# Performance work log

Hardware: AMD Instinct MI355X
Metric: run time of the kernel (lower is better)

Reference implementation:

```python
import jax, jax.numpy as jnp
import numpy as np

B, S, D, E, F = 4, 2048, 1024, 8, 4096


def setup_inputs() -> dict:
    key = jax.random.key(0)
    k1, k2, k3, k4 = jax.random.split(key, 4)
    x = jax.random.normal(k1, (B, S, D), dtype=jnp.float32)
    Wg = jax.random.normal(k2, (D, E), dtype=jnp.float32) / np.sqrt(D).astype(np.float32)
    w1 = jax.random.normal(k3, (E, D, F), dtype=jnp.float32) / np.sqrt(D).astype(np.float32)
    w2 = jax.random.normal(k4, (E, F, D), dtype=jnp.float32) / np.sqrt(F).astype(np.float32)
    return {"x": x, "Wg": Wg, "w1": w1, "w2": w2, "k": 2}


def reference(x, Wg, w1, w2, k):
    # x: [B, S, D] -> flatten tokens
    b, s, d = x.shape
    e = Wg.shape[1]
    xf = x.reshape(-1, d)                      # [T, D]
    t = xf.shape[0]
    logits = xf @ Wg                           # [T, E] gate logits
    topv, topi = jax.lax.top_k(logits, k)      # [T, k]
    # softmax over the top-k logits in float32, cast back (matches torch impl)
    w = jax.nn.softmax(topv.astype(jnp.float32), axis=-1).astype(x.dtype)
    # dense routing matrix [T, E]: weight for selected experts, 0 elsewhere
    route = jnp.zeros((t, e), dtype=x.dtype).at[jnp.arange(t)[:, None], topi].set(w)
    # per-expert FFN: y_e = gelu(x @ w1[e]) @ w2[e]; combine = sum_e route[:,e] * y_e
    out = jnp.zeros_like(xf)
    for ei in range(e):  # small fixed expert count
        h = jax.nn.gelu(xf @ w1[ei])           # [T, F]
        out = out + route[:, ei:ei + 1] * (h @ w2[ei])
    return out.reshape(b, s, d)
```

## Files before the change

kernel.cpp:

```cpp
#include <hip/hip_runtime.h>
#include <stdint.h>

#define T_TOK   8192
#define DMODEL  1024
#define NEXP    8
#define FFN     4096
#define TASSIGN 16384

typedef unsigned short u16;
typedef __attribute__((ext_vector_type(8))) short short8;
typedef __attribute__((ext_vector_type(8))) u16 u16x8;
typedef __attribute__((ext_vector_type(4))) u16 u16x4;
typedef __attribute__((ext_vector_type(4))) float f32x4;

__device__ __forceinline__ float bf2f(u16 u) {
  union { unsigned int i; float f; } v; v.i = ((unsigned int)u) << 16; return v.f;
}
__device__ __forceinline__ u16 f2bf(float f) {
  union { float f; unsigned int i; } v; v.f = f;
  unsigned int x = v.i;
  x += 0x7fffu + ((x >> 16) & 1u);
  return (u16)(x >> 16);
}
__device__ __forceinline__ float gelu_tanh(float x) {
  float z = 0.7978845608028654f * x * (1.0f + 0.044715f * x * x);
  float t = 1.0f - 2.0f / (__expf(2.0f * z) + 1.0f);
  return 0.5f * x * (1.0f + t);
}
__device__ __forceinline__ void async16(const void* g, void* l) {
  __builtin_amdgcn_global_load_lds((__attribute__((address_space(1))) void*)g,
                                   (__attribute__((address_space(3))) void*)l,
                                   16, 0, 0);
}

__global__ void init_kernel(int* __restrict__ meta) {
  if (threadIdx.x < 32) meta[threadIdx.x] = 0;
}

__global__ void gate_kernel(const float* __restrict__ x, const float* __restrict__ Wg,
                            int* __restrict__ topi, float* __restrict__ topw,
                            int* __restrict__ counts, u16* __restrict__ xb) {
  __shared__ float sWg[DMODEL * NEXP];
  int tid = threadIdx.x;
  for (int i = tid; i < DMODEL * NEXP / 4; i += 256)
    ((float4*)sWg)[i] = ((const float4*)Wg)[i];
  __syncthreads();

  int wave = tid >> 6, lane = tid & 63;
  int t = blockIdx.x * 4 + wave;

  float acc[NEXP] = {0, 0, 0, 0, 0, 0, 0, 0};
  const float* xr = x + (size_t)t * DMODEL;
  u16* xbr = xb + (size_t)t * DMODEL;
  for (int d0 = 0; d0 < DMODEL; d0 += 128) {
    int d = d0 + lane * 2;
    float2 xx = *(const float2*)(xr + d);
    *(uint32_t*)(xbr + d) = (uint32_t)f2bf(xx.x) | ((uint32_t)f2bf(xx.y) << 16);
    const float* g0 = sWg + (size_t)d * NEXP;
#pragma unroll
    for (int e = 0; e < NEXP; e++)
      acc[e] += xx.x * g0[e] + xx.y * g0[NEXP + e];
  }
#pragma unroll
  for (int off = 32; off > 0; off >>= 1)
#pragma unroll
    for (int e = 0; e < NEXP; e++)
      acc[e] += __shfl_xor(acc[e], off, 64);

  if (lane == 0) {
    float v0 = -1e30f, v1 = -1e30f; int i0 = 0, i1 = 0;
#pragma unroll
    for (int e = 0; e < NEXP; e++) {
      float v = acc[e];
      if (v > v0) { v1 = v0; i1 = i0; v0 = v; i0 = e; }
      else if (v > v1) { v1 = v; i1 = e; }
    }
    float e1 = __expf(v1 - v0);
    float s = 1.0f / (1.0f + e1);
    topi[t * 2] = i0; topi[t * 2 + 1] = i1;
    topw[t * 2] = s;  topw[t * 2 + 1] = e1 * s;
    atomicAdd(&counts[i0], 1);
    atomicAdd(&counts[i1], 1);
  }
}

__global__ void scan_kernel(const int* __restrict__ counts, int* __restrict__ offsets,
                            int* __restrict__ cursors) {
  if (threadIdx.x == 0) {
    int s = 0;
    for (int e = 0; e < NEXP; e++) { offsets[e] = s; s += counts[e]; }
    offsets[NEXP] = s;
  }
  if (threadIdx.x < NEXP) cursors[threadIdx.x] = 0;
}

__global__ void build_kernel(const int* __restrict__ topi, const int* __restrict__ offsets,
                             int* __restrict__ cursors, int* __restrict__ perm,
                             int* __restrict__ slotrow) {
  int t = blockIdx.x * blockDim.x + threadIdx.x;
  if (t >= T_TOK) return;
#pragma unroll
  for (int s = 0; s < 2; s++) {
    int e = topi[t * 2 + s];
    int p = atomicAdd(&cursors[e], 1);
    int g = offsets[e] + p;
    perm[g] = t;
    slotrow[t * 2 + s] = g;
  }
}

__global__ void transpose_kernel(const float* __restrict__ w1, const float* __restrict__ w2,
                                 u16* __restrict__ w1t, u16* __restrict__ w2t) {
  __shared__ u16 sh[64][72];
  int z = blockIdx.y;
  const float* src; u16* dst; int R, C;
  if (z < 8) { src = w1 + (size_t)z * (DMODEL * FFN); dst = w1t + (size_t)z * (FFN * DMODEL); R = DMODEL; C = FFN; }
  else       { src = w2 + (size_t)(z - 8) * (FFN * DMODEL); dst = w2t + (size_t)(z - 8) * (DMODEL * FFN); R = FFN; C = DMODEL; }
  int tilesC = C >> 6;
  int rt = blockIdx.x / tilesC, ct = blockIdx.x % tilesC;
  int tid = threadIdx.x;
#pragma unroll
  for (int i = 0; i < 2; i++) {
    int idx = i * 256 + tid;
    int r = idx >> 3, c8 = (idx & 7) * 8;
    const float* s = src + (size_t)(rt * 64 + r) * C + ct * 64 + c8;
    float4 v0 = *(const float4*)s, v1 = *(const float4*)(s + 4);
    u16* d = &sh[r][c8];
    d[0] = f2bf(v0.x); d[1] = f2bf(v0.y); d[2] = f2bf(v0.z); d[3] = f2bf(v0.w);
    d[4] = f2bf(v1.x); d[5] = f2bf(v1.y); d[6] = f2bf(v1.z); d[7] = f2bf(v1.w);
  }
  __syncthreads();
#pragma unroll
  for (int i = 0; i < 2; i++) {
    int idx = i * 256 + tid;
    int c = idx >> 3, r8 = (idx & 7) * 8;
    u16x8 v;
#pragma unroll
    for (int j = 0; j < 8; j++) v[j] = sh[r8 + j][c];
    *(u16x8*)(dst + (size_t)(ct * 64 + c) * R + rt * 64 + r8) = v;
  }
}

template <int K, int N, bool GATHER, bool GELU>
__global__ __launch_bounds__(256) void gemm_t_kernel(
    const u16* __restrict__ A, const u16* __restrict__ Bt, u16* __restrict__ C,
    const int* __restrict__ offsets, const int* __restrict__ perm) {
  __shared__ u16 As[128 * 32];
  __shared__ u16 Bs[128 * 32];
  int e = blockIdx.z;
  int off = offsets[e];
  int nrows = offsets[e + 1] - off;
  int mtile = blockIdx.y;
  if (mtile * 128 >= nrows) return;
  int ntile = blockIdx.x;

  int tid = threadIdx.x;
  int wave = tid >> 6, lane = tid & 63;

  int rr = tid >> 2;
  int kc = (tid & 3) * 8;

  int m0 = mtile * 128 + rr;
  int mm0 = min(m0, nrows - 1);
  int mm1 = min(m0 + 64, nrows - 1);
  const u16 *arow0, *arow1;
  if (GATHER) {
    arow0 = A + (size_t)perm[off + mm0] * K + kc;
    arow1 = A + (size_t)perm[off + mm1] * K + kc;
  } else {
    arow0 = A + (size_t)(off + mm0) * K + kc;
    arow1 = A + (size_t)(off + mm1) * K + kc;
  }
  const u16* bbase = Bt + (size_t)e * ((size_t)N * K);
  const u16* brow0 = bbase + (size_t)(ntile * 128 + rr) * K + kc;
  const u16* brow1 = bbase + (size_t)(ntile * 128 + rr + 64) * K + kc;

  u16* asd0 = As + (size_t)(wave * 64) * 8;
  u16* asd1 = As + (size_t)(256 + wave * 64) * 8;
  u16* bsd0 = Bs + (size_t)(wave * 64) * 8;
  u16* bsd1 = Bs + (size_t)(256 + wave * 64) * 8;

  int wm = (wave >> 1) * 64, wn = (wave & 1) * 64;
  int lm = lane & 15, kq = lane >> 4;

  f32x4 acc[4][4];
  f32x4 zero = {0.f, 0.f, 0.f, 0.f};
#pragma unroll
  for (int i = 0; i < 4; i++)
#pragma unroll
    for (int j = 0; j < 4; j++) acc[i][j] = zero;

  for (int k0 = 0; k0 < K; k0 += 32) {
    async16(arow0 + k0, asd0);
    async16(arow1 + k0, asd1);
    async16(brow0 + k0, bsd0);
    async16(brow1 + k0, bsd1);
    __syncthreads();
    short8 a[4], b[4];
#pragma unroll
    for (int i = 0; i < 4; i++) {
      a[i] = *(const short8*)(As + (size_t)(wm + i * 16 + lm) * 32 + kq * 8);
      b[i] = *(const short8*)(Bs + (size_t)(wn + i * 16 + lm) * 32 + kq * 8);
    }
#pragma unroll
    for (int i = 0; i < 4; i++)
#pragma unroll
      for (int j = 0; j < 4; j++)
        acc[i][j] = __builtin_amdgcn_mfma_f32_16x16x32_bf16(a[i], b[j], acc[i][j], 0, 0, 0);
    __syncthreads();
  }

#pragma unroll
  for (int i = 0; i < 4; i++) {
    int rbase = mtile * 128 + wm + i * 16 + kq * 4;
#pragma unroll
    for (int r = 0; r < 4; r++) {
      int row = rbase + r;
      if (row < nrows) {
        u16* crow = C + (size_t)(off + row) * N + ntile * 128 + wn + lm;
#pragma unroll
        for (int j = 0; j < 4; j++) {
          float v = acc[i][j][r];
          if (GELU) v = gelu_tanh(v);
          crow[j * 16] = f2bf(v);
        }
      }
    }
  }
}

template <int K, int N, bool GATHER, bool GELU>
__global__ __launch_bounds__(256) void gemm_f_kernel(
    const u16* __restrict__ A, const float* __restrict__ B, u16* __restrict__ C,
    const int* __restrict__ offsets, const int* __restrict__ perm) {
  __shared__ u16 As[128 * 32];
  __shared__ u16 Bs[128 * 32];
  int e = blockIdx.z;
  int off = offsets[e];
  int nrows = offsets[e + 1] - off;
  int mtile = blockIdx.y;
  if (mtile * 128 >= nrows) return;
  int ntile = blockIdx.x;

  int tid = threadIdx.x;
  int wave = tid >> 6, lane = tid & 63;

  int rr = tid >> 2;
  int kc = (tid & 3) * 8;
  int m0 = mtile * 128 + rr;
  int mm0 = min(m0, nrows - 1);
  int mm1 = min(m0 + 64, nrows - 1);
  const u16 *arow0, *arow1;
  if (GATHER) {
    arow0 = A + (size_t)perm[off + mm0] * K + kc;
    arow1 = A + (size_t)perm[off + mm1] * K + kc;
  } else {
    arow0 = A + (size_t)(off + mm0) * K + kc;
    arow1 = A + (size_t)(off + mm1) * K + kc;
  }

  int kk2 = (tid >> 4) * 2;
  int n8  = (tid & 15) * 8;
  const float* brow0 = B + (size_t)e * ((size_t)K * N) + (size_t)kk2 * N
                         + (size_t)ntile * 128 + n8;
  const float* brow1 = brow0 + N;

  int wm = (wave >> 1) * 64, wn = (wave & 1) * 64;
  int lm = lane & 15, kq = lane >> 4;

  f32x4 acc[4][4];
  f32x4 zero = {0.f, 0.f, 0.f, 0.f};
#pragma unroll
  for (int i = 0; i < 4; i++)
#pragma unroll
    for (int j = 0; j < 4; j++) acc[i][j] = zero;

  uint32_t* bs32 = (uint32_t*)Bs;
  for (int k0 = 0; k0 < K; k0 += 32) {
    u16x8 av0 = *(const u16x8*)(arow0 + k0);
    u16x8 av1 = *(const u16x8*)(arow1 + k0);
    float4 b00 = *(const float4*)(brow0 + (size_t)k0 * N);
    float4 b01 = *(const float4*)(brow0 + (size_t)k0 * N + 4);
    float4 b10 = *(const float4*)(brow1 + (size_t)k0 * N);
    float4 b11 = *(const float4*)(brow1 + (size_t)k0 * N + 4);
    __syncthreads();
    *(u16x8*)(As + (size_t)rr * 32 + kc) = av0;
    *(u16x8*)(As + (size_t)(rr + 64) * 32 + kc) = av1;
    int wcol = kk2 >> 1;
    bs32[(size_t)(n8 + 0) * 16 + wcol] = (uint32_t)f2bf(b00.x) | ((uint32_t)f2bf(b10.x) << 16);
    bs32[(size_t)(n8 + 1) * 16 + wcol] = (uint32_t)f2bf(b00.y) | ((uint32_t)f2bf(b10.y) << 16);
    bs32[(size_t)(n8 + 2) * 16 + wcol] = (uint32_t)f2bf(b00.z) | ((uint32_t)f2bf(b10.z) << 16);
    bs32[(size_t)(n8 + 3) * 16 + wcol] = (uint32_t)f2bf(b00.w) | ((uint32_t)f2bf(b10.w) << 16);
    bs32[(size_t)(n8 + 4) * 16 + wcol] = (uint32_t)f2bf(b01.x) | ((uint32_t)f2bf(b11.x) << 16);
    bs32[(size_t)(n8 + 5) * 16 + wcol] = (uint32_t)f2bf(b01.y) | ((uint32_t)f2bf(b11.y) << 16);
    bs32[(size_t)(n8 + 6) * 16 + wcol] = (uint32_t)f2bf(b01.z) | ((uint32_t)f2bf(b11.z) << 16);
    bs32[(size_t)(n8 + 7) * 16 + wcol] = (uint32_t)f2bf(b01.w) | ((uint32_t)f2bf(b11.w) << 16);
    __syncthreads();
    short8 a[4], b[4];
#pragma unroll
    for (int i = 0; i < 4; i++) {
      a[i] = *(const short8*)(As + (size_t)(wm + i * 16 + lm) * 32 + kq * 8);
      b[i] = *(const short8*)(Bs + (size_t)(wn + i * 16 + lm) * 32 + kq * 8);
    }
#pragma unroll
    for (int i = 0; i < 4; i++)
#pragma unroll
      for (int j = 0; j < 4; j++)
        acc[i][j] = __builtin_amdgcn_mfma_f32_16x16x32_bf16(a[i], b[j], acc[i][j], 0, 0, 0);
  }

#pragma unroll
  for (int i = 0; i < 4; i++) {
    int rbase = mtile * 128 + wm + i * 16 + kq * 4;
#pragma unroll
    for (int r = 0; r < 4; r++) {
      int row = rbase + r;
      if (row < nrows) {
        u16* crow = C + (size_t)(off + row) * N + ntile * 128 + wn + lm;
#pragma unroll
        for (int j = 0; j < 4; j++) {
          float v = acc[i][j][r];
          if (GELU) v = gelu_tanh(v);
          crow[j * 16] = f2bf(v);
        }
      }
    }
  }
}

__global__ void combine_kernel(const u16* __restrict__ Y, const int* __restrict__ slotrow,
                               const float* __restrict__ topw, float* __restrict__ out) {
  int idx = blockIdx.x * 256 + threadIdx.x;
  int t = idx >> 8;
  int c = (idx & 255) * 4;
  int g0 = slotrow[t * 2], g1 = slotrow[t * 2 + 1];
  float w0 = topw[t * 2], w1 = topw[t * 2 + 1];
  u16x4 y0 = *(const u16x4*)(Y + (size_t)g0 * DMODEL + c);
  u16x4 y1 = *(const u16x4*)(Y + (size_t)g1 * DMODEL + c);
  float4 o;
  o.x = w0 * bf2f(y0[0]) + w1 * bf2f(y1[0]);
  o.y = w0 * bf2f(y0[1]) + w1 * bf2f(y1[1]);
  o.z = w0 * bf2f(y0[2]) + w1 * bf2f(y1[2]);
  o.w = w0 * bf2f(y0[3]) + w1 * bf2f(y1[3]);
  *(float4*)(out + (size_t)t * DMODEL + c) = o;
}

extern "C" void kernel_launch(void* const* d_in, const int* in_sizes, int n_in,
                              void* d_out, int out_size, void* d_ws, size_t ws_size,
                              hipStream_t stream) {
  const float* x  = (const float*)d_in[0];
  const float* Wg = (const float*)d_in[1];
  const float* w1 = (const float*)d_in[2];
  const float* w2 = (const float*)d_in[3];
  float* out = (float*)d_out;

  const size_t SZ_H   = (size_t)TASSIGN * FFN * 2;
  const size_t SZ_W1T = (size_t)NEXP * FFN * DMODEL * 2;
  const size_t SZ_W2T = (size_t)NEXP * DMODEL * FFN * 2;
  const size_t SZ_XB  = (size_t)T_TOK * DMODEL * 2;
  const size_t SZ_Y   = (size_t)TASSIGN * DMODEL * 2;
  const size_t SZ_SMALL = (size_t)TASSIGN * 4 * 4 + 4096;
  const size_t WS_FULL = SZ_H + SZ_W1T + SZ_W2T + SZ_XB + SZ_SMALL;

  uint8_t* ws = (uint8_t*)d_ws;
  bool fast = (ws_size >= WS_FULL);

  size_t o = 0;
  u16* H = (u16*)(ws + o); o += SZ_H;
  u16 *w1t = nullptr, *w2t = nullptr, *Y;
  if (fast) {
    w1t = (u16*)(ws + o); o += SZ_W1T;
    w2t = (u16*)(ws + o); o += SZ_W2T;
    Y = w1t;
  } else {
    Y = (u16*)(ws + o); o += SZ_Y;
  }
  u16* xb = (u16*)(ws + o); o += SZ_XB;
  int*   topi    = (int*)(ws + o);   o += (size_t)TASSIGN * 4;
  float* topw    = (float*)(ws + o); o += (size_t)TASSIGN * 4;
  int*   perm    = (int*)(ws + o);   o += (size_t)TASSIGN * 4;
  int*   slotrow = (int*)(ws + o);   o += (size_t)TASSIGN * 4;
  int*   meta    = (int*)(ws + o);
  int* counts = meta, *offsets = meta + 8, *cursors = meta + 17;

  init_kernel<<<1, 64, 0, stream>>>(meta);
  gate_kernel<<<T_TOK / 4, 256, 0, stream>>>(x, Wg, topi, topw, counts, xb);
  scan_kernel<<<1, 64, 0, stream>>>(counts, offsets, cursors);
  build_kernel<<<T_TOK / 256, 256, 0, stream>>>(topi, offsets, cursors, perm, slotrow);

  if (fast) {
    transpose_kernel<<<dim3(1024, 16), 256, 0, stream>>>(w1, w2, w1t, w2t);
    gemm_t_kernel<DMODEL, FFN, true, true>
        <<<dim3(FFN / 128, 64, NEXP), 256, 0, stream>>>(xb, w1t, H, offsets, perm);
    gemm_t_kernel<FFN, DMODEL, false, false>
        <<<dim3(DMODEL / 128, 64, NEXP), 256, 0, stream>>>(H, w2t, Y, offsets, perm);
  } else {
    gemm_f_kernel<DMODEL, FFN, true, true>
        <<<dim3(FFN / 128, 64, NEXP), 256, 0, stream>>>(xb, w1, H, offsets, perm);
    gemm_f_kernel<FFN, DMODEL, false, false>
        <<<dim3(DMODEL / 128, 64, NEXP), 256, 0, stream>>>(H, w2, Y, offsets, perm);
  }
  combine_kernel<<<(T_TOK * DMODEL / 4) / 256, 256, 0, stream>>>(Y, slotrow, topw, out);
}
```

Baseline: 1.041 ms.

## Replace expert GEMM with 256x256 double-buffered pipelined 8-wave kernel

Replaces the 128x128, single-buffered expert GEMM with a 512-thread kernel that computes 256x256 tiles over a K step of 64. Global-to-LDS async loads are double-buffered and interleaved with MFMA phases. LDS is XOR-swizzled to avoid bank conflicts, and s_setprio is raised around the MFMA blocks. The grid is flattened with the expert index in the low bits so experts interleave across CUs. This targets the load-then-sync stall and low arithmetic intensity of the old kernel, at the cost of 128KB of LDS per block, high register pressure and intricate hand scheduling of waitcnt and barriers.

```diff
diff --git a/kernel.cpp b/kernel.cpp
--- a/kernel.cpp
+++ b/kernel.cpp
@@ -142,91 +142,140 @@
 }
 
 template <int K, int N, bool GATHER, bool GELU>
-__global__ __launch_bounds__(256) void gemm_t_kernel(
+__global__ __launch_bounds__(512, 2) void gemm8_kernel(
     const u16* __restrict__ A, const u16* __restrict__ Bt, u16* __restrict__ C,
     const int* __restrict__ offsets, const int* __restrict__ perm) {
-  __shared__ u16 As[128 * 32];
-  __shared__ u16 Bs[128 * 32];
-  int e = blockIdx.z;
+  __shared__ u16 S[65536];
+  constexpr int NTT = N / 256;
+  constexpr int MT  = 32;
+  constexpr int NKT = K / 64;
+
+  int p = blockIdx.x;
+  int e = p & 7;
+  int slot = p >> 3;
+  int ntile = slot / MT;
+  int mtile = slot % MT;
+
   int off = offsets[e];
   int nrows = offsets[e + 1] - off;
-  int mtile = blockIdx.y;
-  if (mtile * 128 >= nrows) return;
-  int ntile = blockIdx.x;
+  if (mtile * 256 >= nrows) return;
 
   int tid = threadIdx.x;
-  int wave = tid >> 6, lane = tid & 63;
-
-  int rr = tid >> 2;
-  int kc = (tid & 3) * 8;
-
-  int m0 = mtile * 128 + rr;
-  int mm0 = min(m0, nrows - 1);
-  int mm1 = min(m0 + 64, nrows - 1);
-  const u16 *arow0, *arow1;
-  if (GATHER) {
-    arow0 = A + (size_t)perm[off + mm0] * K + kc;
-    arow1 = A + (size_t)perm[off + mm1] * K + kc;
-  } else {
-    arow0 = A + (size_t)(off + mm0) * K + kc;
-    arow1 = A + (size_t)(off + mm1) * K + kc;
-  }
+  int w = tid >> 6, l = tid & 63;
+  int lm = l & 15, kq = l >> 4;
+  int warp_m = w >> 2, warp_n = w & 3;
+  int xr = ((l >> 2) & 1) << 4;
+
+  int scol8 = ((l & 7) ^ (((l >> 5) & 1) << 1)) * 8;
+  int rbase = w * 8 + (l >> 3);
+  const u16* aptr[2][2];
+  const u16* bptr[2][2];
   const u16* bbase = Bt + (size_t)e * ((size_t)N * K);
-  const u16* brow0 = bbase + (size_t)(ntile * 128 + rr) * K + kc;
-  const u16* brow1 = bbase + (size_t)(ntile * 128 + rr + 64) * K + kc;
-
-  u16* asd0 = As + (size_t)(wave * 64) * 8;
-  u16* asd1 = As + (size_t)(256 + wave * 64) * 8;
-  u16* bsd0 = Bs + (size_t)(wave * 64) * 8;
-  u16* bsd1 = Bs + (size_t)(256 + wave * 64) * 8;
-
-  int wm = (wave >> 1) * 64, wn = (wave & 1) * 64;
-  int lm = lane & 15, kq = lane >> 4;
-
-  f32x4 acc[4][4];
+#pragma unroll
+  for (int q = 0; q < 2; q++)
+#pragma unroll
+    for (int i = 0; i < 2; i++) {
+      int rr = rbase + i * 64;
+      int rowA = (rr < 64 ? rr : rr + 64) + q * 64;
+      int gm = mtile * 256 + rowA;
+      int gmc = min(gm, nrows - 1);
+      int arow = GATHER ? perm[off + gmc] : (off + gmc);
+      aptr[q][i] = A + (size_t)arow * K + scol8;
+      int rowB = ((rr >> 5) << 6) + (rr & 31) + q * 32;
+      bptr[q][i] = bbase + (size_t)(ntile * 256 + rowB) * K + scol8;
+    }
+  int arb = w * 8;
+  int brb = (w & 3) * 8 + (w >> 2) * 64;
+  u16* As_lds = S;
+  u16* Bs_lds = S + 32768;
+
+#define STAGE_A(q, buf, kt) do {                                                       \
+    async16(aptr[q][0] + (kt) * 64, As_lds + (buf) * 16384 + (arb + (q) * 64) * 64);   \
+    async16(aptr[q][1] + (kt) * 64, As_lds + (buf) * 16384 + (arb + 128 + (q) * 64) * 64); \
+  } while (0)
+#define STAGE_B(q, buf, kt) do {                                                       \
+    async16(bptr[q][0] + (kt) * 64, Bs_lds + (buf) * 16384 + (brb + (q) * 32) * 64);   \
+    async16(bptr[q][1] + (kt) * 64, Bs_lds + (buf) * 16384 + (brb + 128 + (q) * 32) * 64); \
+  } while (0)
+
+  f32x4 acc[8][4];
   f32x4 zero = {0.f, 0.f, 0.f, 0.f};
 #pragma unroll
-  for (int i = 0; i < 4; i++)
+  for (int i = 0; i < 8; i++)
 #pragma unroll
     for (int j = 0; j < 4; j++) acc[i][j] = zero;
 
-  for (int k0 = 0; k0 < K; k0 += 32) {
-    async16(arow0 + k0, asd0);
-    async16(arow1 + k0, asd1);
-    async16(brow0 + k0, bsd0);
-    async16(brow1 + k0, bsd1);
-    __syncthreads();
-    short8 a[4], b[4];
-#pragma unroll
-    for (int i = 0; i < 4; i++) {
-      a[i] = *(const short8*)(As + (size_t)(wm + i * 16 + lm) * 32 + kq * 8);
-      b[i] = *(const short8*)(Bs + (size_t)(wn + i * 16 + lm) * 32 + kq * 8);
-    }
-#pragma unroll
-    for (int i = 0; i < 4; i++)
-#pragma unroll
-      for (int j = 0; j < 4; j++)
-        acc[i][j] = __builtin_amdgcn_mfma_f32_16x16x32_bf16(a[i], b[j], acc[i][j], 0, 0, 0);
-    __syncthreads();
-  }
-
-#pragma unroll
-  for (int i = 0; i < 4; i++) {
-    int rbase = mtile * 128 + wm + i * 16 + kq * 4;
+#define GEMM8_PHASE(BUF, QM, QN, STAGE_STMT, DO_VM)                                    \
+  {                                                                                    \
+    short8 af[4][2], bf[2][2];                                                         \
+    const u16* ab = As_lds + (BUF) * 16384;                                            \
+    const u16* bb = Bs_lds + (BUF) * 16384;                                            \
+    _Pragma("unroll") for (int fi = 0; fi < 4; fi++) {                                 \
+      int ml = warp_m * 128 + ((QM) * 4 + fi) * 16 + lm;                               \
+      _Pragma("unroll") for (int ks = 0; ks < 2; ks++)                                 \
+        af[fi][ks] = *(const short8*)(ab + ((ml * 64 + ks * 32 + kq * 8) ^ xr));       \
+    }                                                                                  \
+    _Pragma("unroll") for (int fj = 0; fj < 2; fj++) {                                 \
+      int nl = warp_n * 64 + ((QN) * 2 + fj) * 16 + lm;                                \
+      _Pragma("unroll") for (int ks = 0; ks < 2; ks++)                                 \
+        bf[fj][ks] = *(const short8*)(bb + ((nl * 64 + ks * 32 + kq * 8) ^ xr));       \
+    }                                                                                  \
+    STAGE_STMT;                                                                        \
+    __builtin_amdgcn_s_barrier();                                                      \
+    asm volatile("s_waitcnt lgkmcnt(0)" ::: "memory");                                 \
+    __builtin_amdgcn_sched_barrier(0);                                                 \
+    __builtin_amdgcn_s_setprio(1);                                                     \
+    _Pragma("unroll") for (int fi = 0; fi < 4; fi++)                                   \
+      _Pragma("unroll") for (int fj = 0; fj < 2; fj++)                                 \
+        _Pragma("unroll") for (int ks = 0; ks < 2; ks++)                               \
+          acc[(QM) * 4 + fi][(QN) * 2 + fj] = __builtin_amdgcn_mfma_f32_16x16x32_bf16( \
+              af[fi][ks], bf[fj][ks], acc[(QM) * 4 + fi][(QN) * 2 + fj], 0, 0, 0);     \
+    __builtin_amdgcn_s_setprio(0);                                                     \
+    if (DO_VM) asm volatile("s_waitcnt vmcnt(4)" ::: "memory");                        \
+    __builtin_amdgcn_s_barrier();                                                      \
+  }
+
+  STAGE_A(0, 0, 0); STAGE_B(0, 0, 0); STAGE_A(1, 0, 0); STAGE_B(1, 0, 0);
+  STAGE_A(0, 1, 1); STAGE_B(0, 1, 1);
+  asm volatile("s_waitcnt vmcnt(4)" ::: "memory");
+  __builtin_amdgcn_s_barrier();
+
+  for (int it = 0; it < NKT / 2; it++) {
+    int kt1 = 2 * it + 1;
+    int t2 = min(2 * it + 2, NKT - 1);
+    int t3 = min(2 * it + 3, NKT - 1);
+    GEMM8_PHASE(0, 0, 0, STAGE_A(1, 1, kt1), 0)
+    GEMM8_PHASE(0, 0, 1, STAGE_B(1, 1, kt1), 0)
+    GEMM8_PHASE(0, 1, 0, STAGE_A(0, 0, t2), 0)
+    GEMM8_PHASE(0, 1, 1, STAGE_B(0, 0, t2), 1)
+    GEMM8_PHASE(1, 0, 0, STAGE_A(1, 0, t2), 0)
+    GEMM8_PHASE(1, 0, 1, STAGE_B(1, 0, t2), 0)
+    GEMM8_PHASE(1, 1, 0, STAGE_A(0, 1, t3), 0)
+    GEMM8_PHASE(1, 1, 1, STAGE_B(0, 1, t3), 1)
+  }
+
+  asm volatile("s_waitcnt vmcnt(0)" ::: "memory");
+
+#pragma unroll
+  for (int fi = 0; fi < 8; fi++) {
+    int rowb = mtile * 256 + warp_m * 128 + fi * 16 + kq * 4;
 #pragma unroll
     for (int r = 0; r < 4; r++) {
-      int row = rbase + r;
+      int row = rowb + r;
       if (row < nrows) {
-        u16* crow = C + (size_t)(off + row) * N + ntile * 128 + wn + lm;
-#pragma unroll
-        for (int j = 0; j < 4; j++) {
-          float v = acc[i][j][r];
+        u16* crow = C + (size_t)(off + row) * N + ntile * 256 + warp_n * 64 + lm;
+#pragma unroll
+        for (int fj = 0; fj < 4; fj++) {
+          float v = acc[fi][fj][r];
           if (GELU) v = gelu_tanh(v);
-          crow[j * 16] = f2bf(v);
+          crow[fj * 16] = f2bf(v);
         }
       }
     }
   }
+#undef STAGE_A
+#undef STAGE_B
+#undef GEMM8_PHASE
 }
 
 template <int K, int N, bool GATHER, bool GELU>
@@ -390,10 +439,10 @@
 
   if (fast) {
     transpose_kernel<<<dim3(1024, 16), 256, 0, stream>>>(w1, w2, w1t, w2t);
-    gemm_t_kernel<DMODEL, FFN, true, true>
-        <<<dim3(FFN / 128, 64, NEXP), 256, 0, stream>>>(xb, w1t, H, offsets, perm);
-    gemm_t_kernel<FFN, DMODEL, false, false>
-        <<<dim3(DMODEL / 128, 64, NEXP), 256, 0, stream>>>(H, w2t, Y, offsets, perm);
+    gemm8_kernel<DMODEL, FFN, true, true>
+        <<<NEXP * (FFN / 256) * 32, 512, 0, stream>>>(xb, w1t, H, offsets, perm);
+    gemm8_kernel<FFN, DMODEL, false, false>
+        <<<NEXP * (DMODEL / 256) * 32, 512, 0, stream>>>(H, w2t, Y, offsets, perm);
   } else {
     gemm_f_kernel<DMODEL, FFN, true, true>
         <<<dim3(FFN / 128, 64, NEXP), 256, 0, stream>>>(xb, w1, H, offsets, perm);
```

New measurement: 1.184 ms. 1.14x slower.

## Swizzle LDS layouts in GEMM and transpose, remap block order across experts

Applied to the files above, without the earlier changes.

Applies XOR swizzles to the shared-memory layouts of the transpose tile and of the GEMM A/B tiles so that LDS writes and reads avoid bank conflicts. The transpose kernel now does one 16-byte vector store per thread instead of scalar stores. The GEMM grid is flattened so that experts are interleaved in the low bits of the block index, with a per-GEMM choice of whether m or n tiles vary fastest, which aims at better L2 reuse and load balance across experts. The risk is that the swizzle math must match between async writes and reads, and the new block order could change cache behaviour in either direction.

```diff
diff --git a/kernel.cpp b/kernel.cpp
--- a/kernel.cpp
+++ b/kernel.cpp
@@ -111,7 +111,7 @@
 
 __global__ void transpose_kernel(const float* __restrict__ w1, const float* __restrict__ w2,
                                  u16* __restrict__ w1t, u16* __restrict__ w2t) {
-  __shared__ u16 sh[64][72];
+  __shared__ u16 sh[64 * 64];
   int z = blockIdx.y;
   const float* src; u16* dst; int R, C;
   if (z < 8) { src = w1 + (size_t)z * (DMODEL * FFN); dst = w1t + (size_t)z * (FFN * DMODEL); R = DMODEL; C = FFN; }
@@ -122,43 +122,52 @@
 #pragma unroll
   for (int i = 0; i < 2; i++) {
     int idx = i * 256 + tid;
-    int r = idx >> 3, c8 = (idx & 7) * 8;
-    const float* s = src + (size_t)(rt * 64 + r) * C + ct * 64 + c8;
+    int r = idx >> 3, c8 = idx & 7;
+    const float* s = src + (size_t)(rt * 64 + r) * C + ct * 64 + c8 * 8;
     float4 v0 = *(const float4*)s, v1 = *(const float4*)(s + 4);
-    u16* d = &sh[r][c8];
-    d[0] = f2bf(v0.x); d[1] = f2bf(v0.y); d[2] = f2bf(v0.z); d[3] = f2bf(v0.w);
-    d[4] = f2bf(v1.x); d[5] = f2bf(v1.y); d[6] = f2bf(v1.z); d[7] = f2bf(v1.w);
+    u16x8 pk;
+    pk[0] = f2bf(v0.x); pk[1] = f2bf(v0.y); pk[2] = f2bf(v0.z); pk[3] = f2bf(v0.w);
+    pk[4] = f2bf(v1.x); pk[5] = f2bf(v1.y); pk[6] = f2bf(v1.z); pk[7] = f2bf(v1.w);
+    *(u16x8*)(sh + r * 64 + ((c8 ^ ((r >> 3) & 7)) * 8)) = pk;
   }
   __syncthreads();
 #pragma unroll
   for (int i = 0; i < 2; i++) {
     int idx = i * 256 + tid;
     int c = idx >> 3, r8 = (idx & 7) * 8;
+    int chunk = (c >> 3) ^ (idx & 7);
     u16x8 v;
 #pragma unroll
-    for (int j = 0; j < 8; j++) v[j] = sh[r8 + j][c];
+    for (int j = 0; j < 8; j++) v[j] = sh[(r8 + j) * 64 + chunk * 8 + (c & 7)];
     *(u16x8*)(dst + (size_t)(ct * 64 + c) * R + rt * 64 + r8) = v;
   }
 }
 
-template <int K, int N, bool GATHER, bool GELU>
+template <int K, int N, bool GATHER, bool GELU, bool NFAST>
 __global__ __launch_bounds__(256) void gemm_t_kernel(
     const u16* __restrict__ A, const u16* __restrict__ Bt, u16* __restrict__ C,
     const int* __restrict__ offsets, const int* __restrict__ perm) {
   __shared__ u16 As[128 * 32];
   __shared__ u16 Bs[128 * 32];
-  int e = blockIdx.z;
+  constexpr int NT = N / 128;
+  constexpr int MT = 64;
+
+  int p = blockIdx.x;
+  int e = p & 7;
+  int slot = p >> 3;
+  int ntile, mtile;
+  if (NFAST) { ntile = slot % NT; mtile = slot / NT; }
+  else       { mtile = slot % MT; ntile = slot / MT; }
+
   int off = offsets[e];
   int nrows = offsets[e + 1] - off;
-  int mtile = blockIdx.y;
   if (mtile * 128 >= nrows) return;
-  int ntile = blockIdx.x;
 
   int tid = threadIdx.x;
   int wave = tid >> 6, lane = tid & 63;
 
   int rr = tid >> 2;
-  int kc = (tid & 3) * 8;
+  int kc = ((tid & 3) ^ ((tid >> 3) & 3)) * 8;
 
   int m0 = mtile * 128 + rr;
   int mm0 = min(m0, nrows - 1);
@@ -182,6 +191,7 @@
 
   int wm = (wave >> 1) * 64, wn = (wave & 1) * 64;
   int lm = lane & 15, kq = lane >> 4;
+  int rdc = (kq ^ ((lm >> 1) & 3)) * 8;
 
   f32x4 acc[4][4];
   f32x4 zero = {0.f, 0.f, 0.f, 0.f};
@@ -199,8 +209,8 @@
     short8 a[4], b[4];
 #pragma unroll
     for (int i = 0; i < 4; i++) {
-      a[i] = *(const short8*)(As + (size_t)(wm + i * 16 + lm) * 32 + kq * 8);
-      b[i] = *(const short8*)(Bs + (size_t)(wn + i * 16 + lm) * 32 + kq * 8);
+      a[i] = *(const short8*)(As + (size_t)(wm + i * 16 + lm) * 32 + rdc);
+      b[i] = *(const short8*)(Bs + (size_t)(wn + i * 16 + lm) * 32 + rdc);
     }
 #pragma unroll
     for (int i = 0; i < 4; i++)
@@ -390,10 +400,10 @@
 
   if (fast) {
     transpose_kernel<<<dim3(1024, 16), 256, 0, stream>>>(w1, w2, w1t, w2t);
-    gemm_t_kernel<DMODEL, FFN, true, true>
-        <<<dim3(FFN / 128, 64, NEXP), 256, 0, stream>>>(xb, w1t, H, offsets, perm);
-    gemm_t_kernel<FFN, DMODEL, false, false>
-        <<<dim3(DMODEL / 128, 64, NEXP), 256, 0, stream>>>(H, w2t, Y, offsets, perm);
+    gemm_t_kernel<DMODEL, FFN, true, true, false>
+        <<<NEXP * (FFN / 128) * 64, 256, 0, stream>>>(xb, w1t, H, offsets, perm);
+    gemm_t_kernel<FFN, DMODEL, false, false, true>
+        <<<NEXP * (DMODEL / 128) * 64, 256, 0, stream>>>(H, w2t, Y, offsets, perm);
   } else {
     gemm_f_kernel<DMODEL, FFN, true, true>
         <<<dim3(FFN / 128, 64, NEXP), 256, 0, stream>>>(xb, w1, H, offsets, perm);
```

Result: faster. 1.015 ms (-2.5%).
